# Kernel optimization log

Measured on AMD Instinct MI355X. Metric: run time of the kernel, lower is better.

The kernel has to match this reference:

```python
import jax, jax.numpy as jnp
import numpy as np
import math

NEG = -1e9  # matches torch masked_fill value -1000000000.0


def setup_inputs() -> dict:
    key = jax.random.key(0)
    k1, k2, k3, k4, k5 = jax.random.split(key, 5)
    N, M, Dk = 32, 2048, 64
    query = jax.random.normal(k1, (N, M, Dk), dtype=jnp.float32)
    key_t = jax.random.normal(k2, (N, M, Dk), dtype=jnp.float32)
    value = jax.random.normal(k3, (N, M, Dk), dtype=jnp.float32)
    key_padding_mask = jax.random.randint(k4, (N, M), 0, 2).astype(bool)
    attn_mask = jax.random.randint(k5, (M, M), 0, 2).astype(bool)
    return {
        "query": query,
        "key": key_t,
        "value": value,
        "key_padding_mask": key_padding_mask,
        "attn_mask": attn_mask,
    }


def reference(query, key, value, key_padding_mask, attn_mask):
    d = query.shape[-1]
    # scores: (N, m, n)
    scores = jnp.einsum("nmd,nkd->nmk", query, key) / math.sqrt(d)
    # key_padding_mask: (N, n) -> broadcast over query dim m
    scores = scores + jnp.where(key_padding_mask, NEG, 0.0)[:, None, :]
    # attn_mask: (m, n) -> broadcast over batch N
    scores = scores + jnp.where(attn_mask, NEG, 0.0)[None, :, :]
    attn_weights = jax.nn.softmax(scores, axis=-1)
    out = jnp.einsum("nmk,nkd->nmd", attn_weights, value)  # dropout p=0.0 is identity
    return out, attn_weights
```

## Files before the change

kernel.cpp:

```cpp
#include <hip/hip_runtime.h>
#include <stdint.h>

typedef __attribute__((ext_vector_type(8))) short v8s;
typedef __attribute__((ext_vector_type(4))) float v4f;

#define NBATCH 32
#define SEQ 2048
#define DHEAD 64

__device__ __forceinline__ unsigned short f2bf(float f) {
  unsigned int x = __float_as_uint(f);
  x += 0x7fffu + ((x >> 16) & 1u);
  return (unsigned short)(x >> 16);
}

__device__ __forceinline__ float bf2f(short s) {
  return __uint_as_float(((unsigned int)(unsigned short)s) << 16);
}

__global__ void cvt_bf16_qk_k(const float* __restrict__ Q, const float* __restrict__ K,
                              unsigned short* __restrict__ Qb,
                              unsigned short* __restrict__ Kb, int n4) {
  int i = blockIdx.x * blockDim.x + threadIdx.x;
  if (i >= n4) return;
  const float* src = blockIdx.y ? K : Q;
  unsigned short* dst = blockIdx.y ? Kb : Qb;
  const float sc = blockIdx.y ? 1.0f : 0.18033688f;
  float4 v = ((const float4*)src)[i];
  ushort4 o;
  o.x = f2bf(v.x * sc); o.y = f2bf(v.y * sc);
  o.z = f2bf(v.z * sc); o.w = f2bf(v.w * sc);
  ((ushort4*)dst)[i] = o;
}

__global__ void vtrans_k(const float* __restrict__ V,
                         unsigned short* __restrict__ Vt) {
  __shared__ float tile[64][65];
  int n = blockIdx.y, k0 = blockIdx.x * 64;
  int t = threadIdx.x;
  int c = t & 63, rb = t >> 6;
#pragma unroll
  for (int it = 0; it < 16; ++it) {
    int r = it * 4 + rb;
    tile[r][c] = V[((size_t)(n * SEQ + k0 + r)) * DHEAD + c];
  }
  __syncthreads();
#pragma unroll
  for (int it = 0; it < 16; ++it) {
    int d = it * 4 + rb;
    Vt[((size_t)(n * DHEAD + d)) * SEQ + k0 + c] = f2bf(tile[c][d]);
  }
}

__global__ void pack_amB_k(const int* __restrict__ am, unsigned int* __restrict__ amB) {
  int tid = blockIdx.x * blockDim.x + threadIdx.x;
  int w = tid & 63, m = tid >> 6;
  unsigned int bits = 0;
#pragma unroll 4
  for (int i = 0; i < 32; ++i)
    bits |= (am[(size_t)m * SEQ + w * 32 + i] != 0 ? 1u : 0u) << i;
  amB[m * 64 + w] = bits;
}

__global__ void pack_kpm_k(const int* __restrict__ kpm, unsigned int* __restrict__ kpmB) {
  int tid = blockIdx.x * blockDim.x + threadIdx.x;
  if (tid >= NBATCH * 64) return;
  int n = tid >> 6, w = tid & 63;
  unsigned int bits = 0;
#pragma unroll 4
  for (int i = 0; i < 32; ++i)
    bits |= (kpm[n * SEQ + w * 32 + i] != 0 ? 1u : 0u) << i;
  kpmB[n * 64 + w] = bits;
}

__global__ __launch_bounds__(512, 4)
void attn_main_k(const unsigned short* __restrict__ Qb,
                 const unsigned short* __restrict__ Kb,
                 const unsigned short* __restrict__ Vt,
                 const unsigned int* __restrict__ amB,
                 const unsigned int* __restrict__ kpmB,
                 float* __restrict__ outO, float* __restrict__ outW) {
  __shared__ __align__(16) char smem[66048];

  const int b = blockIdx.x;
  const int xcd = b & 7, slot = b >> 3;
  const int n = xcd + ((slot >> 7) << 3);
  const int row0 = (slot & 127) * 16;

  const int tid = threadIdx.x;
  const int wave = tid >> 6, lane = tid & 63;
  const int quad = lane >> 4, lq = lane & 15;
  const int colw = wave * 256;

  const unsigned short* qp = Qb + ((size_t)(n * SEQ + row0 + lq)) * DHEAD + quad * 8;
  v8s a0 = *(const v8s*)qp;
  v8s a1 = *(const v8s*)(qp + 32);

  const unsigned int* amRow = amB + (size_t)(row0 + lq) * 64;
  const unsigned int* kpmRow = kpmB + n * 64 + (colw >> 5);

  unsigned int mwv[8];
#pragma unroll
  for (int w2 = 0; w2 < 8; ++w2)
    mwv[w2] = amRow[(colw >> 5) + w2] | kpmRow[w2];

  const unsigned short* kbase =
      Kb + ((size_t)(n * SEQ + colw + lq)) * DHEAD + quad * 8;
  v8s kb0[4], kb1[4];
#pragma unroll
  for (int i = 0; i < 4; ++i) {
    const unsigned short* kp = kbase + (size_t)(i * 16) * DHEAD;
    kb0[i] = *(const v8s*)kp;
    kb1[i] = *(const v8s*)(kp + 32);
  }

  float rsum = 0.f;
#pragma unroll
  for (int kt = 0; kt < 16; ++kt) {
    v8s b0 = kb0[kt & 3], b1 = kb1[kt & 3];
    if (kt < 12) {
      const unsigned short* kp = kbase + (size_t)((kt + 4) * 16) * DHEAD;
      kb0[kt & 3] = *(const v8s*)kp;
      kb1[kt & 3] = *(const v8s*)(kp + 32);
    }
    v4f c = {0.f, 0.f, 0.f, 0.f};
    c = __builtin_amdgcn_mfma_f32_16x16x32_bf16(b0, a0, c, 0, 0, 0);
    c = __builtin_amdgcn_mfma_f32_16x16x32_bf16(b1, a1, c, 0, 0, 0);
    const unsigned int mw = mwv[kt >> 1];
    const int bitbase = (kt & 1) * 16 + quad * 4;
    float e0, e1, e2, e3;
    e0 = (mw >> (bitbase + 0)) & 1u ? 0.f : exp2f(c[0]);
    e1 = (mw >> (bitbase + 1)) & 1u ? 0.f : exp2f(c[1]);
    e2 = (mw >> (bitbase + 2)) & 1u ? 0.f : exp2f(c[2]);
    e3 = (mw >> (bitbase + 3)) & 1u ? 0.f : exp2f(c[3]);
    rsum += (e0 + e1) + (e2 + e3);
    uint2 dd;
    dd.x = ((unsigned int)f2bf(e0)) | (((unsigned int)f2bf(e1)) << 16);
    dd.y = ((unsigned int)f2bf(e2)) | (((unsigned int)f2bf(e3)) << 16);
    const int col0 = colw + kt * 16 + quad * 4;
    *(uint2*)(smem + lq * 4096 +
              ((((col0 >> 3) ^ (lq & 7)) << 4) | ((quad & 1) << 3))) = dd;
  }

  rsum += __shfl_xor(rsum, 16);
  rsum += __shfl_xor(rsum, 32);
  float* wsum = (float*)(smem + 65536);
  if (quad == 0) wsum[wave * 16 + lq] = rsum;
  __syncthreads();

  float rinv[4];
#pragma unroll
  for (int r = 0; r < 4; ++r) {
    float s = 0.f;
#pragma unroll
    for (int w = 0; w < 8; ++w) s += wsum[w * 16 + quad * 4 + r];
    rinv[r] = 1.0f / s;
  }

  {
    float s0 = 0.f, s1 = 0.f;
#pragma unroll
    for (int w = 0; w < 8; ++w) {
      s0 += wsum[w * 16 + wave * 2];
      s1 += wsum[w * 16 + wave * 2 + 1];
    }
    const float rw0 = 1.0f / s0, rw1 = 1.0f / s1;
    float* wbase = outW + ((size_t)(n * SEQ + row0)) * SEQ;
#pragma unroll
    for (int ps = 0; ps < 8; ++ps) {
      const int row = wave * 2 + (ps & 1);
      const float rs = (ps & 1) ? rw1 : rw0;
      const int cb8 = lane + ((ps >> 1) << 6);
      v8s pv = *(const v8s*)(smem + row * 4096 + ((cb8 ^ (row & 7)) << 4));
      v4f f0, f1;
      f0.x = bf2f(pv[0]) * rs; f0.y = bf2f(pv[1]) * rs;
      f0.z = bf2f(pv[2]) * rs; f0.w = bf2f(pv[3]) * rs;
      f1.x = bf2f(pv[4]) * rs; f1.y = bf2f(pv[5]) * rs;
      f1.z = bf2f(pv[6]) * rs; f1.w = bf2f(pv[7]) * rs;
      v4f* dst = (v4f*)(wbase + (size_t)row * SEQ + (cb8 << 3));
      dst[0] = f0;
      dst[1] = f1;
    }
  }

  const unsigned short* vtbase =
      Vt + ((size_t)(n * DHEAD + lq)) * SEQ + colw + quad * 8;
  v4f acc[4] = {{0.f,0.f,0.f,0.f},{0.f,0.f,0.f,0.f},{0.f,0.f,0.f,0.f},{0.f,0.f,0.f,0.f}};
  v8s vb[4];
#pragma unroll
  for (int dt = 0; dt < 4; ++dt)
    vb[dt] = *(const v8s*)(vtbase + (size_t)(dt * 16) * SEQ);
#pragma unroll
  for (int ch = 0; ch < 8; ++ch) {
    const int cb = colw + ch * 32;
    v8s ap = *(const v8s*)(smem + lq * 4096 + (((((cb >> 3) + quad) ^ (lq & 7)) << 4)));
#pragma unroll
    for (int dt = 0; dt < 4; ++dt) {
      v8s bp = vb[dt];
      if (ch < 7)
        vb[dt] = *(const v8s*)(vtbase + (size_t)(dt * 16) * SEQ + (ch + 1) * 32);
      acc[dt] = __builtin_amdgcn_mfma_f32_16x16x32_bf16(ap, bp, acc[dt], 0, 0, 0);
    }
  }
  __syncthreads();

  float* olds = (float*)smem;
#pragma unroll
  for (int dt = 0; dt < 4; ++dt)
#pragma unroll
    for (int r = 0; r < 4; ++r)
      olds[wave * 1088 + (quad * 4 + r) * 68 + dt * 16 + lq] = acc[dt][r] * rinv[r];
  __syncthreads();
#pragma unroll
  for (int s = 0; s < 2; ++s) {
    int e = tid + s * 512;
    int row = e >> 6, d = e & 63;
    float a = 0.f;
#pragma unroll
    for (int w = 0; w < 8; ++w) a += olds[w * 1088 + row * 68 + d];
    outO[((size_t)(n * SEQ + row0 + row)) * DHEAD + d] = a;
  }
}

extern "C" void kernel_launch(void* const* d_in, const int* in_sizes, int n_in,
                              void* d_out, int out_size, void* d_ws, size_t ws_size,
                              hipStream_t stream) {
  const float* Q = (const float*)d_in[0];
  const float* K = (const float*)d_in[1];
  const float* V = (const float*)d_in[2];
  const int* kpm = (const int*)d_in[3];
  const int* am = (const int*)d_in[4];

  float* outO = (float*)d_out;
  float* outW = outO + (size_t)NBATCH * SEQ * DHEAD;

  char* ws = (char*)d_ws;
  unsigned short* Qb = (unsigned short*)ws;
  unsigned short* Kb = (unsigned short*)(ws + (8u << 20));
  unsigned short* Vt = (unsigned short*)(ws + (16u << 20));
  unsigned int* amB = (unsigned int*)(ws + (24u << 20));
  unsigned int* kpmB = (unsigned int*)(ws + (24u << 20) + (1u << 19));

  const int n4 = NBATCH * SEQ * DHEAD / 4;
  cvt_bf16_qk_k<<<dim3(n4 / 256, 2), 256, 0, stream>>>(Q, K, Qb, Kb, n4);
  vtrans_k<<<dim3(SEQ / 64, NBATCH), 256, 0, stream>>>(V, Vt);
  pack_amB_k<<<(SEQ * 64) / 256, 256, 0, stream>>>(am, amB);
  pack_kpm_k<<<8, 256, 0, stream>>>(kpm, kpmB);
  attn_main_k<<<NBATCH * (SEQ / 16), 512, 0, stream>>>(Qb, Kb, Vt, amB, kpmB,
                                                       outO, outW);
}
```

Before: 816.6 us.

## Split fused attention kernel into QK, weight-expand and PV kernels

Splits the single fused attention kernel into three launches. The first computes masked exponentials and writes them as bf16 to a global buffer along with row sums. The second expands that buffer into normalized fp32 attention weights, and the third reads it back to do the PV matmul. This decouples the stages, which may let each run at its own occupancy, but it adds a large bf16 probability round trip through global memory plus extra launches.

After: 949.5 us. 1.16x slower.

```diff
diff --git a/kernel.cpp b/kernel.cpp
--- a/kernel.cpp
+++ b/kernel.cpp
@@ -73,13 +73,13 @@
   kpmB[n * 64 + w] = bits;
 }
 
+
 __global__ __launch_bounds__(512, 4)
-void attn_main_k(const unsigned short* __restrict__ Qb,
-                 const unsigned short* __restrict__ Kb,
-                 const unsigned short* __restrict__ Vt,
-                 const unsigned int* __restrict__ amB,
-                 const unsigned int* __restrict__ kpmB,
-                 float* __restrict__ outO, float* __restrict__ outW) {
+void qk_k(const unsigned short* __restrict__ Qb,
+          const unsigned short* __restrict__ Kb,
+          const unsigned int* __restrict__ amB,
+          const unsigned int* __restrict__ kpmB,
+          unsigned short* __restrict__ Pg, float* __restrict__ Wsum) {
   __shared__ __align__(16) char smem[66048];
 
   const int b = blockIdx.x;
@@ -98,7 +98,6 @@
 
   const unsigned int* amRow = amB + (size_t)(row0 + lq) * 64;
   const unsigned int* kpmRow = kpmB + n * 64 + (colw >> 5);
-
   unsigned int mwv[8];
 #pragma unroll
   for (int w2 = 0; w2 < 8; ++w2)
@@ -148,63 +147,76 @@
   if (quad == 0) wsum[wave * 16 + lq] = rsum;
   __syncthreads();
 
-  float rinv[4];
-#pragma unroll
-  for (int r = 0; r < 4; ++r) {
+  unsigned short* pbase = Pg + ((size_t)(n * SEQ + row0)) * SEQ;
+#pragma unroll
+  for (int ps = 0; ps < 8; ++ps) {
+    const int row = wave * 2 + (ps & 1);
+    const int cb8 = lane + ((ps >> 1) << 6);
+    v8s pv = *(const v8s*)(smem + row * 4096 + ((cb8 ^ (row & 7)) << 4));
+    *(v8s*)(pbase + (size_t)row * SEQ + (cb8 << 3)) = pv;
+  }
+
+  if (tid < 16) {
     float s = 0.f;
 #pragma unroll
-    for (int w = 0; w < 8; ++w) s += wsum[w * 16 + quad * 4 + r];
-    rinv[r] = 1.0f / s;
-  }
-
-  {
-    float s0 = 0.f, s1 = 0.f;
-#pragma unroll
-    for (int w = 0; w < 8; ++w) {
-      s0 += wsum[w * 16 + wave * 2];
-      s1 += wsum[w * 16 + wave * 2 + 1];
-    }
-    const float rw0 = 1.0f / s0, rw1 = 1.0f / s1;
-    float* wbase = outW + ((size_t)(n * SEQ + row0)) * SEQ;
-#pragma unroll
-    for (int ps = 0; ps < 8; ++ps) {
-      const int row = wave * 2 + (ps & 1);
-      const float rs = (ps & 1) ? rw1 : rw0;
-      const int cb8 = lane + ((ps >> 1) << 6);
-      v8s pv = *(const v8s*)(smem + row * 4096 + ((cb8 ^ (row & 7)) << 4));
-      v4f f0, f1;
-      f0.x = bf2f(pv[0]) * rs; f0.y = bf2f(pv[1]) * rs;
-      f0.z = bf2f(pv[2]) * rs; f0.w = bf2f(pv[3]) * rs;
-      f1.x = bf2f(pv[4]) * rs; f1.y = bf2f(pv[5]) * rs;
-      f1.z = bf2f(pv[6]) * rs; f1.w = bf2f(pv[7]) * rs;
-      v4f* dst = (v4f*)(wbase + (size_t)row * SEQ + (cb8 << 3));
-      dst[0] = f0;
-      dst[1] = f1;
-    }
-  }
-
+    for (int w = 0; w < 8; ++w) s += wsum[w * 16 + tid];
+    Wsum[(size_t)n * SEQ + row0 + tid] = s;
+  }
+}
+
+__global__ void expand_k(const unsigned short* __restrict__ Pg,
+                         const float* __restrict__ Wsum,
+                         float* __restrict__ outW) {
+  const int bid = blockIdx.x;
+  const float rinv = 1.0f / Wsum[bid];
+  v8s pv = *(const v8s*)(Pg + (size_t)bid * SEQ + threadIdx.x * 8);
+  float* dst = outW + (size_t)bid * SEQ + threadIdx.x * 8;
+  v4f f0, f1;
+  f0.x = bf2f(pv[0]) * rinv; f0.y = bf2f(pv[1]) * rinv;
+  f0.z = bf2f(pv[2]) * rinv; f0.w = bf2f(pv[3]) * rinv;
+  f1.x = bf2f(pv[4]) * rinv; f1.y = bf2f(pv[5]) * rinv;
+  f1.z = bf2f(pv[6]) * rinv; f1.w = bf2f(pv[7]) * rinv;
+  ((v4f*)dst)[0] = f0;
+  ((v4f*)dst)[1] = f1;
+}
+
+__global__ __launch_bounds__(512)
+void pv_k(const unsigned short* __restrict__ Pg,
+          const unsigned short* __restrict__ Vt,
+          const float* __restrict__ Wsum, float* __restrict__ outO) {
+  __shared__ __align__(16) float olds[8 * 1088];
+
+  const int b = blockIdx.x;
+  const int xcd = b & 7, slot = b >> 3;
+  const int n = xcd + ((slot >> 7) << 3);
+  const int row0 = (slot & 127) * 16;
+
+  const int tid = threadIdx.x;
+  const int wave = tid >> 6, lane = tid & 63;
+  const int quad = lane >> 4, lq = lane & 15;
+  const int colw = wave * 256;
+
+  const unsigned short* prow = Pg + ((size_t)(n * SEQ + row0 + lq)) * SEQ;
   const unsigned short* vtbase =
       Vt + ((size_t)(n * DHEAD + lq)) * SEQ + colw + quad * 8;
+
   v4f acc[4] = {{0.f,0.f,0.f,0.f},{0.f,0.f,0.f,0.f},{0.f,0.f,0.f,0.f},{0.f,0.f,0.f,0.f}};
-  v8s vb[4];
-#pragma unroll
-  for (int dt = 0; dt < 4; ++dt)
-    vb[dt] = *(const v8s*)(vtbase + (size_t)(dt * 16) * SEQ);
 #pragma unroll
   for (int ch = 0; ch < 8; ++ch) {
     const int cb = colw + ch * 32;
-    v8s ap = *(const v8s*)(smem + lq * 4096 + (((((cb >> 3) + quad) ^ (lq & 7)) << 4)));
+    v8s ap = *(const v8s*)(prow + cb + quad * 8);
 #pragma unroll
     for (int dt = 0; dt < 4; ++dt) {
-      v8s bp = vb[dt];
-      if (ch < 7)
-        vb[dt] = *(const v8s*)(vtbase + (size_t)(dt * 16) * SEQ + (ch + 1) * 32);
+      v8s bp = *(const v8s*)(vtbase + (size_t)(dt * 16) * SEQ + ch * 32);
       acc[dt] = __builtin_amdgcn_mfma_f32_16x16x32_bf16(ap, bp, acc[dt], 0, 0, 0);
     }
   }
-  __syncthreads();
-
-  float* olds = (float*)smem;
+
+  float rinv[4];
+#pragma unroll
+  for (int r = 0; r < 4; ++r)
+    rinv[r] = 1.0f / Wsum[(size_t)n * SEQ + row0 + quad * 4 + r];
+
 #pragma unroll
   for (int dt = 0; dt < 4; ++dt)
 #pragma unroll
@@ -240,12 +252,15 @@
   unsigned short* Vt = (unsigned short*)(ws + (16u << 20));
   unsigned int* amB = (unsigned int*)(ws + (24u << 20));
   unsigned int* kpmB = (unsigned int*)(ws + (24u << 20) + (1u << 19));
+  float* Wsum = (float*)(ws + (25u << 20));
+  unsigned short* Pg = (unsigned short*)(ws + (32u << 20));
 
   const int n4 = NBATCH * SEQ * DHEAD / 4;
   cvt_bf16_qk_k<<<dim3(n4 / 256, 2), 256, 0, stream>>>(Q, K, Qb, Kb, n4);
   vtrans_k<<<dim3(SEQ / 64, NBATCH), 256, 0, stream>>>(V, Vt);
   pack_amB_k<<<(SEQ * 64) / 256, 256, 0, stream>>>(am, amB);
   pack_kpm_k<<<8, 256, 0, stream>>>(kpm, kpmB);
-  attn_main_k<<<NBATCH * (SEQ / 16), 512, 0, stream>>>(Qb, Kb, Vt, amB, kpmB,
-                                                       outO, outW);
-}
+  qk_k<<<NBATCH * (SEQ / 16), 512, 0, stream>>>(Qb, Kb, amB, kpmB, Pg, Wsum);
+  expand_k<<<NBATCH * SEQ, 256, 0, stream>>>(Pg, Wsum, outW);
+  pv_k<<<NBATCH * (SEQ / 16), 512, 0, stream>>>(Pg, Vt, Wsum, outO);
+}
```
